# Performance work log

Measured on AMD Instinct MI355X. Metric: run time of the kernel, lower is better.

Reference implementation:

```python
import jax, jax.numpy as jnp
import numpy as np

N_NODES = 100000

def _sage_conv(x, edge_index, w_l, b_l, w_r):
    """PyG SAGEConv with mean aggregation:
    out = lin_l(mean_{j in N(i)} x_j) + lin_r(x_i), bias only on lin_l."""
    src, dst = edge_index[0], edge_index[1]
    msgs = x[src]  # [E, d] gather
    agg = jax.ops.segment_sum(msgs, dst, num_segments=N_NODES)  # [N, d]
    cnt = jax.ops.segment_sum(jnp.ones((edge_index.shape[1],), x.dtype), dst,
                              num_segments=N_NODES)
    agg = agg / jnp.maximum(cnt, 1.0)[:, None]  # mean over neighbors
    return agg @ w_l.T + b_l + x @ w_r.T


def setup_inputs() -> dict:
    key = jax.random.key(0)
    ks = jax.random.split(key, 8)
    in_dim, hid_dim, out_dim = 128, 128, 128
    N, E = N_NODES, 1600000
    x = jax.random.normal(ks[0], (N, in_dim), dtype=jnp.float32)
    edge_index = jax.random.randint(ks[1], (2, E), 0, N, dtype=jnp.int64)
    s = 1.0 / np.sqrt(in_dim)
    w1_l = jax.random.uniform(ks[2], (hid_dim, in_dim), jnp.float32, -s, s)
    w1_r = jax.random.uniform(ks[3], (hid_dim, in_dim), jnp.float32, -s, s)
    b1 = jnp.zeros((hid_dim,), jnp.float32)
    s2 = 1.0 / np.sqrt(hid_dim)
    w2_l = jax.random.uniform(ks[4], (out_dim, hid_dim), jnp.float32, -s2, s2)
    w2_r = jax.random.uniform(ks[5], (out_dim, hid_dim), jnp.float32, -s2, s2)
    b2 = jnp.zeros((out_dim,), jnp.float32)
    return {"x": x, "edge_index": edge_index,
            "w1_l": w1_l, "b1": b1, "w1_r": w1_r,
            "w2_l": w2_l, "b2": b2, "w2_r": w2_r}


def reference(x, edge_index, w1_l, b1, w1_r, w2_l, b2, w2_r):
    h = jax.nn.relu(_sage_conv(x, edge_index, w1_l, b1, w1_r))
    # dropout rate 0.0 -> identity (eval-mode reference)
    out = _sage_conv(h, edge_index, w2_l, b2, w2_r)
    return out
```

## Files before the change

kernel.cpp:

```cpp
#include <hip/hip_runtime.h>

#define NDIM 128
#define BKT_SHIFT 9
#define BKT_NODES 512
#define BKT_CAP   12288
#define PART_CHUNK 4096

typedef unsigned short u16;
typedef unsigned char u8;
typedef unsigned int u32;
typedef __attribute__((ext_vector_type(8))) short bf16x8;
typedef __attribute__((ext_vector_type(4))) float f32x4;
typedef __attribute__((ext_vector_type(2))) float f32x2;

__device__ inline u16 f2bf(float f) {
    u32 u = __float_as_uint(f);
    u += 0x7fffu + ((u >> 16) & 1u);
    return (u16)(u >> 16);
}
__device__ inline float bf2f(u16 h) { return __uint_as_float((u32)h << 16); }

__device__ inline u8 f2q(float f) {
    u32 u = __float_as_uint(f);
    u32 s = (u >> 24) & 0x80u;
    float a = __uint_as_float(u & 0x7fffffffu);
    if (a < 0.015625f)
        return (u8)(s | (u32)__float2int_rn(a * 512.f));
    if (a >= 448.f) return (u8)(s | 0x7Eu);
    u32 ur = (u & 0x7fffffffu) + 0x7FFFFu + ((u >> 20) & 1u);
    int e = (int)(ur >> 23) - 127;
    u32 man = (ur >> 20) & 7u;
    u32 r = ((u32)(e + 7) << 3) | man;
    if (r > 0x7Eu) r = 0x7Eu;
    return (u8)(s | r);
}

#if __has_builtin(__builtin_amdgcn_cvt_pk_f32_fp8)
template<bool HI>
__device__ inline f32x2 dq2(u32 w) {
    return __builtin_amdgcn_cvt_pk_f32_fp8((int)w, HI);
}
#else
__device__ inline float dq1(u32 b) {
    int e = (b >> 3) & 15, m = b & 7, s = (b >> 7) & 1;
    int norm = e ? 1 : 0;
    float f = (float)(m + (norm << 3));
    float sc = __uint_as_float((u32)(((e ? e : 1) - 10) + 127) << 23);
    float v = f * sc;
    return s ? -v : v;
}
template<bool HI>
__device__ inline f32x2 dq2(u32 w) {
    u32 sh = HI ? 16 : 0;
    f32x2 r; r.x = dq1((w >> sh) & 0xff); r.y = dq1((w >> (sh + 8)) & 0xff);
    return r;
}
#endif


__global__ __launch_bounds__(256) void partition_kernel(
    const int* __restrict__ ei, int E,
    int* __restrict__ gcur, u32* __restrict__ ebuf) {
    __shared__ int hcnt[256];
    __shared__ int hbase[256];
    const int tid = threadIdx.x;
    const int base = blockIdx.x * PART_CHUNK;
    hcnt[tid] = 0;
    __syncthreads();

    u32 val[16];
    int bkt[16];
    #pragma unroll
    for (int k = 0; k < 16; ++k) {
        int e = base + k * 256 + tid;
        bkt[k] = -1;
        if (e < E) {
            int src = ei[e];
            int dst = ei[(size_t)E + e];
            int b = dst >> BKT_SHIFT;
            bkt[k] = b;
            val[k] = ((u32)src << BKT_SHIFT) | (u32)(dst & (BKT_NODES - 1));
            atomicAdd(&hcnt[b], 1);
        }
    }
    __syncthreads();
    {
        int c = hcnt[tid];
        if (c > 0) hbase[tid] = atomicAdd(&gcur[tid], c);
        hcnt[tid] = 0;
    }
    __syncthreads();
    #pragma unroll
    for (int k = 0; k < 16; ++k) {
        if (bkt[k] >= 0) {
            int b = bkt[k];
            int r = atomicAdd(&hcnt[b], 1);
            int off = hbase[b] + r;
            if (off < BKT_CAP)
                ebuf[(size_t)b * BKT_CAP + off] = val[k];
        }
    }
}

__global__ __launch_bounds__(256) void bucket_csr_kernel(
    const int* __restrict__ gcur, const u32* __restrict__ ebuf,
    int* __restrict__ row_beg, int* __restrict__ degN,
    int* __restrict__ col, int n) {
    __shared__ int deg_l[BKT_NODES];
    __shared__ int pre_l[BKT_NODES];
    __shared__ int cur_l[BKT_NODES];
    __shared__ int wsum[4];
    const int tid = threadIdx.x;
    const int lane = tid & 63, wid = tid >> 6;
    const int b = blockIdx.x;
    const int node0 = b << BKT_SHIFT;
    int cnt = gcur[b];
    if (cnt > BKT_CAP) cnt = BKT_CAP;
    const size_t ebase = (size_t)b * BKT_CAP;

    deg_l[tid] = 0; deg_l[tid + 256] = 0;
    cur_l[tid] = 0; cur_l[tid + 256] = 0;
    __syncthreads();

    for (int i = tid; i < cnt; i += 256)
        atomicAdd(&deg_l[ebuf[ebase + i] & (BKT_NODES - 1)], 1);
    __syncthreads();

    int v0 = deg_l[2 * tid], v1 = deg_l[2 * tid + 1];
    int s = v0 + v1, inc = s;
    #pragma unroll
    for (int d = 1; d < 64; d <<= 1) {
        int t = __shfl_up(inc, d, 64);
        if (lane >= d) inc += t;
    }
    if (lane == 63) wsum[wid] = inc;
    __syncthreads();
    int woff = 0;
    for (int w = 0; w < wid; ++w) woff += wsum[w];
    int ex = woff + (inc - s);
    pre_l[2 * tid] = ex;
    pre_l[2 * tid + 1] = ex + v0;
    __syncthreads();

    #pragma unroll
    for (int p = 0; p < 2; ++p) {
        int idx = tid + p * 256;
        int node = node0 + idx;
        if (node < n) {
            row_beg[node] = (int)ebase + pre_l[idx];
            degN[node]    = deg_l[idx];
        }
    }

    for (int i = tid; i < cnt; i += 256) {
        u32 v = ebuf[ebase + i];
        int d = v & (BKT_NODES - 1);
        int r = atomicAdd(&cur_l[d], 1);
        col[ebase + pre_l[d] + r] = (int)(v >> BKT_SHIFT);
    }
}


__global__ void build_wt_kernel(const float* __restrict__ wl,
                                const float* __restrict__ wr,
                                u16* __restrict__ wth, u16* __restrict__ wtl) {
    int idx = blockIdx.x * blockDim.x + threadIdx.x;
    if (idx >= 128 * 256) return;
    int o = idx >> 8, k = idx & 255;
    float v = (k < 128) ? wl[o * 128 + k] : wr[o * 128 + (k - 128)];
    u16 hi = f2bf(v);
    wth[idx] = hi;
    wtl[idx] = f2bf(v - bf2f(hi));
}


__global__ __launch_bounds__(256) void to_conv_kernel(
    const float* __restrict__ in, u16* __restrict__ outh,
    u8* __restrict__ outq, int n4) {
    int stride = gridDim.x * blockDim.x;
    for (int i = blockIdx.x * blockDim.x + threadIdx.x; i < n4; i += stride) {
        float4 v = *(const float4*)&in[(size_t)i * 4];
        ushort4 o;
        o.x = f2bf(v.x); o.y = f2bf(v.y); o.z = f2bf(v.z); o.w = f2bf(v.w);
        *(ushort4*)&outh[(size_t)i * 4] = o;
        u32 q = (u32)f2q(v.x) | ((u32)f2q(v.y) << 8) |
                ((u32)f2q(v.z) << 16) | ((u32)f2q(v.w) << 24);
        *(u32*)&outq[(size_t)i * 4] = q;
    }
}


__device__ inline void accumq(float acc[8], uint2 u) {
    f32x2 a;
    a = dq2<false>(u.x); acc[0] += a.x; acc[1] += a.y;
    a = dq2<true >(u.x); acc[2] += a.x; acc[3] += a.y;
    a = dq2<false>(u.y); acc[4] += a.x; acc[5] += a.y;
    a = dq2<true >(u.y); acc[6] += a.x; acc[7] += a.y;
}

__global__ __launch_bounds__(256) void aggregate_fp8_kernel(
    const u8* __restrict__ feat, const int* __restrict__ row_beg,
    const int* __restrict__ degN, const int* __restrict__ col,
    u16* __restrict__ aggh, int n) {
    int node = blockIdx.x * 16 + (threadIdx.x >> 4);
    if (node >= n) return;
    int l = threadIdx.x & 15;
    int beg = row_beg[node];
    int dg  = degN[node];
    int end = beg + dg;
    float acc[8] = {0.f, 0.f, 0.f, 0.f, 0.f, 0.f, 0.f, 0.f};
    int j = beg;
    for (; j + 8 <= end; j += 8) {
        int s[8];
        #pragma unroll
        for (int q = 0; q < 8; ++q) s[q] = col[j + q];
        uint2 u[8];
        #pragma unroll
        for (int q = 0; q < 8; ++q)
            u[q] = *(const uint2*)&feat[(size_t)s[q] * NDIM + l * 8];
        #pragma unroll
        for (int q = 0; q < 8; ++q) accumq(acc, u[q]);
    }
    if (j + 4 <= end) {
        int s[4];
        #pragma unroll
        for (int q = 0; q < 4; ++q) s[q] = col[j + q];
        uint2 u[4];
        #pragma unroll
        for (int q = 0; q < 4; ++q)
            u[q] = *(const uint2*)&feat[(size_t)s[q] * NDIM + l * 8];
        #pragma unroll
        for (int q = 0; q < 4; ++q) accumq(acc, u[q]);
        j += 4;
    }
    for (; j < end; ++j) {
        uint2 u = *(const uint2*)&feat[(size_t)col[j] * NDIM + l * 8];
        accumq(acc, u);
    }
    float inv = (dg > 0) ? 1.0f / (float)dg : 0.f;
    u16 hs[8];
    #pragma unroll
    for (int q = 0; q < 8; ++q) hs[q] = f2bf(acc[q] * inv);
    *(ushort4*)&aggh[(size_t)node * NDIM + l * 8]     = make_ushort4(hs[0], hs[1], hs[2], hs[3]);
    *(ushort4*)&aggh[(size_t)node * NDIM + l * 8 + 4] = make_ushort4(hs[4], hs[5], hs[6], hs[7]);
}


__global__ __launch_bounds__(256, 1) void gemm_bstat_kernel(
    const u16* __restrict__ aggh, const u16* __restrict__ selfh,
    const u16* __restrict__ wth, const u16* __restrict__ wtl,
    const float* __restrict__ bias,
    float* __restrict__ outF, u16* __restrict__ outH, u8* __restrict__ outQ,
    int M, int do_relu) {
    const int lane = threadIdx.x & 63;
    const int wid  = threadIdx.x >> 6;
    const int rr = lane & 15, kb = lane >> 4;
    const int c0 = wid * 32;
    const int ntiles = (M + 31) / 32;

    bf16x8 BH[2][8], BL[2][8];
    #pragma unroll
    for (int nt = 0; nt < 2; ++nt) {
        const u16* bh = &wth[(size_t)(c0 + nt * 16 + rr) * 256];
        const u16* bl = &wtl[(size_t)(c0 + nt * 16 + rr) * 256];
        #pragma unroll
        for (int ks = 0; ks < 8; ++ks) {
            BH[nt][ks] = *(const bf16x8*)&bh[ks * 32 + kb * 8];
            BL[nt][ks] = *(const bf16x8*)&bl[ks * 32 + kb * 8];
        }
    }
    const float bb0 = bias[c0 + rr];
    const float bb1 = bias[c0 + 16 + rr];

    for (int t = blockIdx.x; t < ntiles; t += gridDim.x) {
        const int r0 = t * 32;
        bf16x8 A[2][8];
        #pragma unroll
        for (int mt = 0; mt < 2; ++mt) {
            int row = r0 + mt * 16 + rr;
            if (row >= M) row = M - 1;
            const u16* ag = &aggh[(size_t)row * NDIM];
            const u16* sf = &selfh[(size_t)row * NDIM];
            #pragma unroll
            for (int ks = 0; ks < 4; ++ks) A[mt][ks]     = *(const bf16x8*)&ag[ks * 32 + kb * 8];
            #pragma unroll
            for (int ks = 0; ks < 4; ++ks) A[mt][4 + ks] = *(const bf16x8*)&sf[ks * 32 + kb * 8];
        }
        f32x4 acc[2][2];
        #pragma unroll
        for (int mt = 0; mt < 2; ++mt)
            #pragma unroll
            for (int nt = 0; nt < 2; ++nt)
                acc[mt][nt] = (f32x4){0.f, 0.f, 0.f, 0.f};
        #pragma unroll
        for (int ks = 0; ks < 8; ++ks)
            #pragma unroll
            for (int mt = 0; mt < 2; ++mt)
                #pragma unroll
                for (int nt = 0; nt < 2; ++nt) {
                    acc[mt][nt] = __builtin_amdgcn_mfma_f32_16x16x32_bf16(A[mt][ks], BH[nt][ks], acc[mt][nt], 0, 0, 0);
                    acc[mt][nt] = __builtin_amdgcn_mfma_f32_16x16x32_bf16(A[mt][ks], BL[nt][ks], acc[mt][nt], 0, 0, 0);
                }
        #pragma unroll
        for (int mt = 0; mt < 2; ++mt) {
            #pragma unroll
            for (int r = 0; r < 4; ++r) {
                int grow = r0 + mt * 16 + kb * 4 + r;
                if (grow < M) {
                    float v0 = acc[mt][0][r] + bb0;
                    float v1 = acc[mt][1][r] + bb1;
                    if (do_relu) { v0 = fmaxf(v0, 0.f); v1 = fmaxf(v1, 0.f); }
                    if (outF) {
                        outF[(size_t)grow * NDIM + c0 + rr]      = v0;
                        outF[(size_t)grow * NDIM + c0 + 16 + rr] = v1;
                    }
                    if (outH) {
                        outH[(size_t)grow * NDIM + c0 + rr]      = f2bf(v0);
                        outH[(size_t)grow * NDIM + c0 + 16 + rr] = f2bf(v1);
                    }
                    if (outQ) {
                        outQ[(size_t)grow * NDIM + c0 + rr]      = f2q(v0);
                        outQ[(size_t)grow * NDIM + c0 + 16 + rr] = f2q(v1);
                    }
                }
            }
        }
    }
}


extern "C" void kernel_launch(void* const* d_in, const int* in_sizes, int n_in,
                              void* d_out, int out_size, void* d_ws, size_t ws_size,
                              hipStream_t stream) {
    const float* x    = (const float*)d_in[0];
    const int*   ei   = (const int*)d_in[1];
    const float* w1_l = (const float*)d_in[2];
    const float* b1   = (const float*)d_in[3];
    const float* w1_r = (const float*)d_in[4];
    const float* w2_l = (const float*)d_in[5];
    const float* b2   = (const float*)d_in[6];
    const float* w2_r = (const float*)d_in[7];
    const int N = in_sizes[0] / NDIM;
    const int E = in_sizes[1] / 2;
    float* out = (float*)d_out;

    const int NB = (N + BKT_NODES - 1) >> BKT_SHIFT;

    char* ws = (char*)d_ws;
    size_t off = 0;
    auto take = [&](size_t bytes) -> char* {
        char* p = ws + off;
        off += (bytes + 255) & ~(size_t)255;
        return p;
    };
    int* row_beg = (int*)take((size_t)N * 4);
    int* degN    = (int*)take((size_t)N * 4);
    int* gcur    = (int*)take((size_t)NB * 4);
    u32* ebuf    = (u32*)take((size_t)NB * BKT_CAP * 4);
    int* colA    = (int*)take((size_t)NB * BKT_CAP * 4);
    u16* wt1h    = (u16*)take(128 * 256 * 2);
    u16* wt1l    = (u16*)take(128 * 256 * 2);
    u16* wt2h    = (u16*)take(128 * 256 * 2);
    u16* wt2l    = (u16*)take(128 * 256 * 2);
    u16* aggh    = (u16*)take((size_t)N * NDIM * 2);
    u16* hh      = (u16*)take((size_t)N * NDIM * 2);
    u16* xh = (u16*)d_out;
    u8*  xq = (u8*)d_out + (size_t)N * NDIM * 2;
    u8*  hq = (u8*)d_out + (size_t)N * NDIM * 3;

    (void)hipMemsetAsync(gcur, 0, (size_t)NB * 4, stream);
    partition_kernel<<<(E + PART_CHUNK - 1) / PART_CHUNK, 256, 0, stream>>>(ei, E, gcur, ebuf);
    bucket_csr_kernel<<<NB, 256, 0, stream>>>(gcur, ebuf, row_beg, degN, colA, N);
    build_wt_kernel<<<128, 256, 0, stream>>>(w1_l, w1_r, wt1h, wt1l);
    build_wt_kernel<<<128, 256, 0, stream>>>(w2_l, w2_r, wt2h, wt2l);
    to_conv_kernel<<<2048, 256, 0, stream>>>(x, xh, xq, N * NDIM / 4);

    const int gblk = 512;
    aggregate_fp8_kernel<<<(N + 15) / 16, 256, 0, stream>>>(xq, row_beg, degN, colA, aggh, N);
    gemm_bstat_kernel<<<gblk, 256, 0, stream>>>(aggh, xh, wt1h, wt1l, b1,
                                                (float*)0, hh, hq, N, 1);
    aggregate_fp8_kernel<<<(N + 15) / 16, 256, 0, stream>>>(hq, row_beg, degN, colA, aggh, N);
    gemm_bstat_kernel<<<gblk, 256, 0, stream>>>(aggh, hh, wt2h, wt2l, b2,
                                                out, (u16*)0, (u8*)0, N, 0);
}
```

Baseline: 223.7 us.

## Double-buffer A tiles in persistent GEMM with 16-row tiles

The persistent GEMM kernel now works on 16-row tiles instead of 32-row tiles and software-pipelines the activation loads. It keeps two register buffers so the next tile's A fragments load while the MFMAs for the current tile run. Empty asm statements pin the weight and A registers so the compiler cannot sink or merge the loads. The aim is to hide global-load latency in this memory-bound GEMM, at the cost of higher register pressure and less work per tile.

```diff
diff --git a/kernel.cpp b/kernel.cpp
--- a/kernel.cpp
+++ b/kernel.cpp
@@ -256,75 +256,94 @@
     const int wid  = threadIdx.x >> 6;
     const int rr = lane & 15, kb = lane >> 4;
     const int c0 = wid * 32;
-    const int ntiles = (M + 31) / 32;
-
-    bf16x8 BH[2][8], BL[2][8];
-    #pragma unroll
-    for (int nt = 0; nt < 2; ++nt) {
-        const u16* bh = &wth[(size_t)(c0 + nt * 16 + rr) * 256];
-        const u16* bl = &wtl[(size_t)(c0 + nt * 16 + rr) * 256];
+    const int ntiles = (M + 15) / 16;
+    const int stride = gridDim.x;
+
+    bf16x8 BH0[8], BL0[8], BH1[8], BL1[8];
+    {
+        const u16* bh0 = &wth[(size_t)(c0 + rr) * 256];
+        const u16* bl0 = &wtl[(size_t)(c0 + rr) * 256];
+        const u16* bh1 = &wth[(size_t)(c0 + 16 + rr) * 256];
+        const u16* bl1 = &wtl[(size_t)(c0 + 16 + rr) * 256];
         #pragma unroll
         for (int ks = 0; ks < 8; ++ks) {
-            BH[nt][ks] = *(const bf16x8*)&bh[ks * 32 + kb * 8];
-            BL[nt][ks] = *(const bf16x8*)&bl[ks * 32 + kb * 8];
-        }
+            BH0[ks] = *(const bf16x8*)&bh0[ks * 32 + kb * 8];
+            BL0[ks] = *(const bf16x8*)&bl0[ks * 32 + kb * 8];
+            BH1[ks] = *(const bf16x8*)&bh1[ks * 32 + kb * 8];
+            BL1[ks] = *(const bf16x8*)&bl1[ks * 32 + kb * 8];
+        }
+        #pragma unroll
+        for (int ks = 0; ks < 8; ++ks)
+            asm volatile("" : "+v"(BH0[ks]), "+v"(BL0[ks]),
+                              "+v"(BH1[ks]), "+v"(BL1[ks]));
     }
     const float bb0 = bias[c0 + rr];
     const float bb1 = bias[c0 + 16 + rr];
 
-    for (int t = blockIdx.x; t < ntiles; t += gridDim.x) {
-        const int r0 = t * 32;
-        bf16x8 A[2][8];
-        #pragma unroll
-        for (int mt = 0; mt < 2; ++mt) {
-            int row = r0 + mt * 16 + rr;
-            if (row >= M) row = M - 1;
-            const u16* ag = &aggh[(size_t)row * NDIM];
-            const u16* sf = &selfh[(size_t)row * NDIM];
-            #pragma unroll
-            for (int ks = 0; ks < 4; ++ks) A[mt][ks]     = *(const bf16x8*)&ag[ks * 32 + kb * 8];
-            #pragma unroll
-            for (int ks = 0; ks < 4; ++ks) A[mt][4 + ks] = *(const bf16x8*)&sf[ks * 32 + kb * 8];
-        }
-        f32x4 acc[2][2];
-        #pragma unroll
-        for (int mt = 0; mt < 2; ++mt)
-            #pragma unroll
-            for (int nt = 0; nt < 2; ++nt)
-                acc[mt][nt] = (f32x4){0.f, 0.f, 0.f, 0.f};
-        #pragma unroll
-        for (int ks = 0; ks < 8; ++ks)
-            #pragma unroll
-            for (int mt = 0; mt < 2; ++mt)
-                #pragma unroll
-                for (int nt = 0; nt < 2; ++nt) {
-                    acc[mt][nt] = __builtin_amdgcn_mfma_f32_16x16x32_bf16(A[mt][ks], BH[nt][ks], acc[mt][nt], 0, 0, 0);
-                    acc[mt][nt] = __builtin_amdgcn_mfma_f32_16x16x32_bf16(A[mt][ks], BL[nt][ks], acc[mt][nt], 0, 0, 0);
+    auto loadA = [&](bf16x8* A, int t) {
+        int row = t * 16 + rr;
+        if (row >= M) row = M - 1;
+        const u16* ag = &aggh[(size_t)row * NDIM];
+        const u16* sf = &selfh[(size_t)row * NDIM];
+        #pragma unroll
+        for (int ks = 0; ks < 4; ++ks) A[ks]     = *(const bf16x8*)&ag[ks * 32 + kb * 8];
+        #pragma unroll
+        for (int ks = 0; ks < 4; ++ks) A[4 + ks] = *(const bf16x8*)&sf[ks * 32 + kb * 8];
+    };
+    auto pinA = [&](bf16x8* A) {
+        #pragma unroll
+        for (int i = 0; i < 8; ++i) asm volatile("" : "+v"(A[i]));
+    };
+    auto computeStore = [&](bf16x8* A, int t) {
+        f32x4 acc0 = (f32x4){0.f, 0.f, 0.f, 0.f};
+        f32x4 acc1 = (f32x4){0.f, 0.f, 0.f, 0.f};
+        #pragma unroll
+        for (int ks = 0; ks < 8; ++ks) {
+            acc0 = __builtin_amdgcn_mfma_f32_16x16x32_bf16(A[ks], BH0[ks], acc0, 0, 0, 0);
+            acc0 = __builtin_amdgcn_mfma_f32_16x16x32_bf16(A[ks], BL0[ks], acc0, 0, 0, 0);
+            acc1 = __builtin_amdgcn_mfma_f32_16x16x32_bf16(A[ks], BH1[ks], acc1, 0, 0, 0);
+            acc1 = __builtin_amdgcn_mfma_f32_16x16x32_bf16(A[ks], BL1[ks], acc1, 0, 0, 0);
+        }
+        #pragma unroll
+        for (int r = 0; r < 4; ++r) {
+            int grow = t * 16 + kb * 4 + r;
+            if (grow < M) {
+                float v0 = acc0[r] + bb0;
+                float v1 = acc1[r] + bb1;
+                if (do_relu) { v0 = fmaxf(v0, 0.f); v1 = fmaxf(v1, 0.f); }
+                if (outF) {
+                    outF[(size_t)grow * NDIM + c0 + rr]      = v0;
+                    outF[(size_t)grow * NDIM + c0 + 16 + rr] = v1;
                 }
-        #pragma unroll
-        for (int mt = 0; mt < 2; ++mt) {
-            #pragma unroll
-            for (int r = 0; r < 4; ++r) {
-                int grow = r0 + mt * 16 + kb * 4 + r;
-                if (grow < M) {
-                    float v0 = acc[mt][0][r] + bb0;
-                    float v1 = acc[mt][1][r] + bb1;
-                    if (do_relu) { v0 = fmaxf(v0, 0.f); v1 = fmaxf(v1, 0.f); }
-                    if (outF) {
-                        outF[(size_t)grow * NDIM + c0 + rr]      = v0;
-                        outF[(size_t)grow * NDIM + c0 + 16 + rr] = v1;
-                    }
-                    if (outH) {
-                        outH[(size_t)grow * NDIM + c0 + rr]      = f2bf(v0);
-                        outH[(size_t)grow * NDIM + c0 + 16 + rr] = f2bf(v1);
-                    }
-                    if (outQ) {
-                        outQ[(size_t)grow * NDIM + c0 + rr]      = f2q(v0);
-                        outQ[(size_t)grow * NDIM + c0 + 16 + rr] = f2q(v1);
-                    }
+                if (outH) {
+                    outH[(size_t)grow * NDIM + c0 + rr]      = f2bf(v0);
+                    outH[(size_t)grow * NDIM + c0 + 16 + rr] = f2bf(v1);
+                }
+                if (outQ) {
+                    outQ[(size_t)grow * NDIM + c0 + rr]      = f2q(v0);
+                    outQ[(size_t)grow * NDIM + c0 + 16 + rr] = f2q(v1);
                 }
             }
         }
+    };
+
+    bf16x8 A0[8], A1[8];
+    int t = blockIdx.x;
+    if (t >= ntiles) return;
+    loadA(A0, t);
+    while (true) {
+        int tn = t + stride;
+        pinA(A0);
+        if (tn < ntiles) loadA(A1, tn);
+        computeStore(A0, t);
+        t = tn;
+        if (t >= ntiles) break;
+        tn = t + stride;
+        pinA(A1);
+        if (tn < ntiles) loadA(A0, tn);
+        computeStore(A1, t);
+        t = tn;
+        if (t >= ntiles) break;
     }
 }
 
```

Result: faster. 210.8 us (-5.8%).
